# Kernel optimization log

Measured on AMD Instinct MI355X. Metric: run time of the kernel, lower is better.

The kernel has to match this reference:

```python
import jax, jax.numpy as jnp
import numpy as np

B, T, C = 32, 256, 512
MAX_LEN = 25


def setup_inputs() -> dict:
    key = jax.random.key(0)
    ks = jax.random.split(key, 6)
    scale = 1.0 / np.sqrt(C)
    return {
        "word_features": jax.random.normal(ks[0], (B, T, C), dtype=jnp.float32),
        "word_fc_w": jax.random.normal(ks[1], (C, C), dtype=jnp.float32) * scale,
        "word_fc_b": jax.random.normal(ks[2], (C,), dtype=jnp.float32) * scale,
        "pos_emb": jax.random.normal(ks[3], (MAX_LEN, C), dtype=jnp.float32),
        "atten_w": jax.random.normal(ks[4], (C,), dtype=jnp.float32) * scale,
        "atten_b": jax.random.normal(ks[5], (1,), dtype=jnp.float32) * scale,
    }


def reference(word_features, word_fc_w, word_fc_b, pos_emb, atten_w, atten_b):
    # word_fc: (b,t,c) -> (b,t,c)
    wf = jnp.einsum("btc,dc->btd", word_features, word_fc_w) + word_fc_b
    # additive (Bahdanau) attention scores over t for each of max_len query positions
    # add_features: (b, L, t, c) = wf[:,None,:,:] + pos_emb[None,:,None,:]
    add_features = jnp.tanh(wf[:, None, :, :] + pos_emb[None, :, None, :])
    # atten_fc: (b, L, t, 1) -> squeeze -> (b, L, t)
    scores = jnp.einsum("bltc,c->blt", add_features, atten_w) + atten_b[0]
    attn = jax.nn.softmax(scores, axis=2)  # softmax over t
    # bmm: (b,L,t) @ (b,t,c) -> (b,L,c)
    pvam_features = jnp.einsum("blt,btc->blc", attn, wf)
    return pvam_features
```

## Files before the change

### kernel.cpp

```cpp
#include <hip/hip_runtime.h>

#define Bn 32
#define Tn 256
#define Cn 512
#define Ln 25

typedef _Float16 h8 __attribute__((ext_vector_type(8)));
typedef _Float16 h4 __attribute__((ext_vector_type(4)));
typedef __attribute__((ext_vector_type(4))) float f32x4;

#define SCALE2LOG2E 2.885390081777927f

#if __has_builtin(__builtin_amdgcn_exp2f)
#define EXP2(x) __builtin_amdgcn_exp2f(x)
#else
#define EXP2(x) __expf(0.69314718056f * (x))
#endif

#define DPP_ADD(v, ctrl) \
    ((v) + __int_as_float(__builtin_amdgcn_update_dpp(0, __float_as_int(v), ctrl, 0xf, 0xf, true)))

__device__ __forceinline__ float tanh_fast(float x) {
    float e = EXP2(SCALE2LOG2E * x);
    return fmaf(-2.f, __builtin_amdgcn_rcpf(1.f + e), 1.f);
}

#define NA_OCT (Bn * Tn * Cn / 8)
#define NW_OCT (Cn * Cn / 8)
#define NP_OCT (Ln * Cn / 8)
__global__ __launch_bounds__(256) void k_convert(
        const float* __restrict__ A, const float* __restrict__ W,
        const float* __restrict__ pos,
        _Float16* __restrict__ A2, _Float16* __restrict__ W2,
        float* __restrict__ TP) {
    int idx = blockIdx.x * 256 + threadIdx.x;
    if (idx < NA_OCT + NW_OCT) {
        const float* src;
        _Float16* dst;
        int off;
        if (idx < NA_OCT) { src = A; dst = A2; off = idx * 8; }
        else              { src = W; dst = W2; off = (idx - NA_OCT) * 8; }
        float4 v0 = *(const float4*)&src[off];
        float4 v1 = *(const float4*)&src[off + 4];
        h8 o;
        o[0] = (_Float16)v0.x; o[1] = (_Float16)v0.y;
        o[2] = (_Float16)v0.z; o[3] = (_Float16)v0.w;
        o[4] = (_Float16)v1.x; o[5] = (_Float16)v1.y;
        o[6] = (_Float16)v1.z; o[7] = (_Float16)v1.w;
        *(h8*)&dst[off] = o;
    } else if (idx < NA_OCT + NW_OCT + NP_OCT) {
        int off = (idx - NA_OCT - NW_OCT) * 8;
        float4 v0 = *(const float4*)&pos[off];
        float4 v1 = *(const float4*)&pos[off + 4];
        float4 t0, t1;
        t0.x = tanh_fast(v0.x); t0.y = tanh_fast(v0.y);
        t0.z = tanh_fast(v0.z); t0.w = tanh_fast(v0.w);
        t1.x = tanh_fast(v1.x); t1.y = tanh_fast(v1.y);
        t1.z = tanh_fast(v1.z); t1.w = tanh_fast(v1.w);
        *(float4*)&TP[off] = t0;
        *(float4*)&TP[off + 4] = t1;
    }
}

#define BM 128
#define BN 64
#define BKg 64
__global__ __launch_bounds__(256) void k_gemm(
        const _Float16* __restrict__ A2, const _Float16* __restrict__ W2,
        const float* __restrict__ bias, _Float16* __restrict__ wf) {
    __shared__ _Float16 As[BM * BKg];
    __shared__ _Float16 Ws[BN * BKg];
    const int tid  = threadIdx.x;
    const int lane = tid & 63;
    const int wv   = tid >> 6;
    const int m0 = blockIdx.y * BM;
    const int n0 = blockIdx.x * BN;
    const int wm = (wv >> 1) * 64;
    const int wn = (wv & 1) * 32;
    const int r = lane & 15, q = lane >> 4;

    const _Float16* gA[4];
    const _Float16* gW[2];
    #pragma unroll
    for (int rr = 0; rr < 4; ++rr) {
        int p = rr * 256 + tid;
        int row = p >> 3, pk = p & 7;
        int lk = pk ^ (row & 7);
        gA[rr] = A2 + (size_t)(m0 + row) * Cn + lk * 8;
    }
    #pragma unroll
    for (int rr = 0; rr < 2; ++rr) {
        int p = rr * 256 + tid;
        int row = p >> 3, pk = p & 7;
        int lk = pk ^ (row & 7);
        gW[rr] = W2 + (size_t)(n0 + row) * Cn + lk * 8;
    }

    f32x4 acc[4][2];
    #pragma unroll
    for (int mi = 0; mi < 4; ++mi)
        #pragma unroll
        for (int ni = 0; ni < 2; ++ni) acc[mi][ni] = (f32x4){0.f, 0.f, 0.f, 0.f};

    for (int kt = 0; kt < Cn / BKg; ++kt) {
        __syncthreads();
        #pragma unroll
        for (int rr = 0; rr < 4; ++rr) {
            __builtin_amdgcn_global_load_lds(
                (const __attribute__((address_space(1))) unsigned int*)gA[rr],
                (__attribute__((address_space(3))) unsigned int*)(As + (rr * 256 + wv * 64) * 8),
                16, 0, 0);
            gA[rr] += BKg;
        }
        #pragma unroll
        for (int rr = 0; rr < 2; ++rr) {
            __builtin_amdgcn_global_load_lds(
                (const __attribute__((address_space(1))) unsigned int*)gW[rr],
                (__attribute__((address_space(3))) unsigned int*)(Ws + (rr * 256 + wv * 64) * 8),
                16, 0, 0);
            gW[rr] += BKg;
        }
        __syncthreads();

        h8 af[4][2], bfr[2][2];
        #pragma unroll
        for (int mi = 0; mi < 4; ++mi)
            #pragma unroll
            for (int kk = 0; kk < 2; ++kk) {
                int row = wm + mi * 16 + r;
                int phys = (kk * 4 + q) ^ (r & 7);
                af[mi][kk] = *(const h8*)&As[row * BKg + phys * 8];
            }
        #pragma unroll
        for (int ni = 0; ni < 2; ++ni)
            #pragma unroll
            for (int kk = 0; kk < 2; ++kk) {
                int row = wn + ni * 16 + r;
                int phys = (kk * 4 + q) ^ (r & 7);
                bfr[ni][kk] = *(const h8*)&Ws[row * BKg + phys * 8];
            }
        #pragma unroll
        for (int kk = 0; kk < 2; ++kk)
            #pragma unroll
            for (int mi = 0; mi < 4; ++mi)
                #pragma unroll
                for (int ni = 0; ni < 2; ++ni)
                    acc[mi][ni] = __builtin_amdgcn_mfma_f32_16x16x32_f16(
                        af[mi][kk], bfr[ni][kk], acc[mi][ni], 0, 0, 0);
    }

    #pragma unroll
    for (int ni = 0; ni < 2; ++ni) {
        const float bv = bias[n0 + wn + ni * 16 + r];
        #pragma unroll
        for (int mi = 0; mi < 4; ++mi)
            #pragma unroll
            for (int reg = 0; reg < 4; ++reg) {
                int row = m0 + wm + mi * 16 + q * 4 + reg;
                int col = n0 + wn + ni * 16 + r;
                wf[(size_t)row * Cn + col] = (_Float16)(acc[mi][ni][reg] + bv);
            }
    }
}

__global__ __launch_bounds__(512) void k_scores(
        const _Float16* __restrict__ wf, const float* __restrict__ TP,
        const float* __restrict__ aw, float* __restrict__ scores) {
    __shared__ float part[4 * Ln * 8];
    const int tid  = threadIdx.x;
    const int lane = tid & 63;
    const int wv   = tid >> 6;
    const int tl   = wv >> 1;
    const int ch   = wv & 1;
    const int t    = blockIdx.x * 4 + tl;
    const int b    = blockIdx.y;
    const int co   = ch * 256 + lane * 4;

    const h4 wh = *(const h4*)&wf[(size_t)(b * Tn + t) * Cn + co];
    float4 tw;
    tw.x = tanh_fast((float)wh[0]); tw.y = tanh_fast((float)wh[1]);
    tw.z = tanh_fast((float)wh[2]); tw.w = tanh_fast((float)wh[3]);
    const float4 a = *(const float4*)&aw[co];

    const float* pp = TP + co;
    float* prt = &part[tl * Ln * 8 + ch * 4 + (lane >> 4)];
    const bool writer = ((lane & 15) == 0);

    #pragma unroll
    for (int lo = 0; lo < 5; ++lo) {
        float4 pv[5];
        #pragma unroll
        for (int j = 0; j < 5; ++j)
            pv[j] = *(const float4*)(pp + (lo * 5 + j) * Cn);
        #pragma unroll
        for (int j = 0; j < 5; ++j) {
            const float4 p = pv[j];
            float s;
            {
                float d = fmaf(tw.x, p.x, 1.f);
                s = a.x * (tw.x + p.x) * __builtin_amdgcn_rcpf(d);
            }
            {
                float d = fmaf(tw.y, p.y, 1.f);
                s = fmaf(a.y * (tw.y + p.y), __builtin_amdgcn_rcpf(d), s);
            }
            {
                float d = fmaf(tw.z, p.z, 1.f);
                s = fmaf(a.z * (tw.z + p.z), __builtin_amdgcn_rcpf(d), s);
            }
            {
                float d = fmaf(tw.w, p.w, 1.f);
                s = fmaf(a.w * (tw.w + p.w), __builtin_amdgcn_rcpf(d), s);
            }
            s = DPP_ADD(s, 0xB1);
            s = DPP_ADD(s, 0x4E);
            s = DPP_ADD(s, 0x141);
            s = DPP_ADD(s, 0x140);
            if (writer) prt[(lo * 5 + j) * 8] = s;
        }
    }
    __syncthreads();
    if (tid < 4 * Ln) {
        int tl2 = tid / Ln, l2 = tid - tl2 * Ln;
        const float* q = &part[(tl2 * Ln + l2) * 8];
        float v = ((q[0] + q[1]) + (q[2] + q[3])) + ((q[4] + q[5]) + (q[6] + q[7]));
        scores[(b * Ln + l2) * Tn + blockIdx.x * 4 + tl2] = v;
    }
}

__global__ __launch_bounds__(512) void k_pvam(
        const _Float16* __restrict__ wf, const float* __restrict__ scores,
        float* __restrict__ out) {
    __shared__ float buf[8 * Ln * 64];
    __shared__ float pT[Tn][28];
    const int tid = threadIdx.x;
    const int cx  = blockIdx.x;
    const int b   = blockIdx.y;

    const float* sc = scores + b * Ln * Tn;
    for (int i = tid * 4; i < Ln * Tn; i += 2048)
        *(float4*)&buf[i] = *(const float4*)&sc[i];
    __syncthreads();

    const int lane = tid & 63;
    const int wv   = tid >> 6;

    for (int l = wv; l < Ln; l += 8) {
        float v0 = buf[l * Tn + lane];
        float v1 = buf[l * Tn + 64 + lane];
        float v2 = buf[l * Tn + 128 + lane];
        float v3 = buf[l * Tn + 192 + lane];
        float m = fmaxf(fmaxf(v0, v1), fmaxf(v2, v3));
        #pragma unroll
        for (int o = 32; o > 0; o >>= 1) m = fmaxf(m, __shfl_xor(m, o));
        float e0 = __expf(v0 - m), e1 = __expf(v1 - m);
        float e2 = __expf(v2 - m), e3 = __expf(v3 - m);
        float s = e0 + e1 + e2 + e3;
        #pragma unroll
        for (int o = 32; o > 0; o >>= 1) s += __shfl_xor(s, o);
        float rs = __builtin_amdgcn_rcpf(s);
        pT[lane][l]       = e0 * rs;
        pT[64 + lane][l]  = e1 * rs;
        pT[128 + lane][l] = e2 * rs;
        pT[192 + lane][l] = e3 * rs;
    }
    __syncthreads();

    const int c = cx * 64 + lane;
    float acc[Ln];
    #pragma unroll
    for (int l = 0; l < Ln; ++l) acc[l] = 0.f;

    const _Float16* wfp = wf + (size_t)(b * Tn + wv * 32) * Cn + c;
    for (int tt = 0; tt < 32; ++tt) {
        float w = (float)wfp[(size_t)tt * Cn];
        const float* pp = &pT[wv * 32 + tt][0];
        float p[Ln];
        *(float4*)&p[0]  = *(const float4*)&pp[0];
        *(float4*)&p[4]  = *(const float4*)&pp[4];
        *(float4*)&p[8]  = *(const float4*)&pp[8];
        *(float4*)&p[12] = *(const float4*)&pp[12];
        *(float4*)&p[16] = *(const float4*)&pp[16];
        *(float4*)&p[20] = *(const float4*)&pp[20];
        p[24] = pp[24];
        #pragma unroll
        for (int l = 0; l < Ln; ++l) acc[l] = fmaf(p[l], w, acc[l]);
    }

    __syncthreads();
    #pragma unroll
    for (int l = 0; l < Ln; ++l)
        buf[(wv * Ln + l) * 64 + lane] = acc[l];
    __syncthreads();
    for (int idx = tid; idx < Ln * 64; idx += 512) {
        int l = idx >> 6, cc = idx & 63;
        float v = 0.f;
        #pragma unroll
        for (int w = 0; w < 8; ++w) v += buf[(w * Ln + l) * 64 + cc];
        out[(b * Ln + l) * Cn + cx * 64 + cc] = v;
    }
}

extern "C" void kernel_launch(void* const* d_in, const int* in_sizes, int n_in,
                              void* d_out, int out_size, void* d_ws, size_t ws_size,
                              hipStream_t stream) {
    const float* A    = (const float*)d_in[0];
    const float* W    = (const float*)d_in[1];
    const float* bias = (const float*)d_in[2];
    const float* pos  = (const float*)d_in[3];
    const float* aw   = (const float*)d_in[4];

    char* ws = (char*)d_ws;
    _Float16*  wf     = (_Float16*)ws;
    float*     scores = (float*)(ws + 8388608ull);
    _Float16*  A2     = (_Float16*)(ws + 9240576ull);
    _Float16*  W2     = (_Float16*)(ws + 17629184ull);
    float*     TP     = (float*)(ws + 18153472ull);
    float* out = (float*)d_out;

    const int nconv = (NA_OCT + NW_OCT + NP_OCT + 255) / 256;
    k_convert<<<nconv, 256, 0, stream>>>(A, W, pos, A2, W2, TP);
    k_gemm<<<dim3(Cn / BN, (Bn * Tn) / BM), 256, 0, stream>>>(A2, W2, bias, wf);
    k_scores<<<dim3(Tn / 4, Bn), 512, 0, stream>>>(wf, TP, aw, scores);
    k_pvam<<<dim3(Cn / 64, Bn), 512, 0, stream>>>(wf, scores, out);
}
```

Baseline: 121.8 us.

## Fuse fp32-to-fp16 activation conversion into GEMM and simplify tanh-sum algebra

```diff
diff --git a/kernel.cpp b/kernel.cpp
--- a/kernel.cpp
+++ b/kernel.cpp
@@ -20,45 +20,33 @@
 #define DPP_ADD(v, ctrl) \
     ((v) + __int_as_float(__builtin_amdgcn_update_dpp(0, __float_as_int(v), ctrl, 0xf, 0xf, true)))
 
-__device__ __forceinline__ float tanh_fast(float x) {
-    float e = EXP2(SCALE2LOG2E * x);
-    return fmaf(-2.f, __builtin_amdgcn_rcpf(1.f + e), 1.f);
-}
-
-#define NA_OCT (Bn * Tn * Cn / 8)
 #define NW_OCT (Cn * Cn / 8)
 #define NP_OCT (Ln * Cn / 8)
 __global__ __launch_bounds__(256) void k_convert(
-        const float* __restrict__ A, const float* __restrict__ W,
-        const float* __restrict__ pos,
-        _Float16* __restrict__ A2, _Float16* __restrict__ W2,
-        float* __restrict__ TP) {
+        const float* __restrict__ W, const float* __restrict__ pos,
+        _Float16* __restrict__ W2, float* __restrict__ EP) {
     int idx = blockIdx.x * 256 + threadIdx.x;
-    if (idx < NA_OCT + NW_OCT) {
-        const float* src;
-        _Float16* dst;
-        int off;
-        if (idx < NA_OCT) { src = A; dst = A2; off = idx * 8; }
-        else              { src = W; dst = W2; off = (idx - NA_OCT) * 8; }
-        float4 v0 = *(const float4*)&src[off];
-        float4 v1 = *(const float4*)&src[off + 4];
+    if (idx < NW_OCT) {
+        int off = idx * 8;
+        float4 v0 = *(const float4*)&W[off];
+        float4 v1 = *(const float4*)&W[off + 4];
         h8 o;
         o[0] = (_Float16)v0.x; o[1] = (_Float16)v0.y;
         o[2] = (_Float16)v0.z; o[3] = (_Float16)v0.w;
         o[4] = (_Float16)v1.x; o[5] = (_Float16)v1.y;
         o[6] = (_Float16)v1.z; o[7] = (_Float16)v1.w;
-        *(h8*)&dst[off] = o;
-    } else if (idx < NA_OCT + NW_OCT + NP_OCT) {
-        int off = (idx - NA_OCT - NW_OCT) * 8;
+        *(h8*)&W2[off] = o;
+    } else if (idx < NW_OCT + NP_OCT) {
+        int off = (idx - NW_OCT) * 8;
         float4 v0 = *(const float4*)&pos[off];
         float4 v1 = *(const float4*)&pos[off + 4];
         float4 t0, t1;
-        t0.x = tanh_fast(v0.x); t0.y = tanh_fast(v0.y);
-        t0.z = tanh_fast(v0.z); t0.w = tanh_fast(v0.w);
-        t1.x = tanh_fast(v1.x); t1.y = tanh_fast(v1.y);
-        t1.z = tanh_fast(v1.z); t1.w = tanh_fast(v1.w);
-        *(float4*)&TP[off] = t0;
-        *(float4*)&TP[off + 4] = t1;
+        t0.x = EXP2(SCALE2LOG2E * v0.x); t0.y = EXP2(SCALE2LOG2E * v0.y);
+        t0.z = EXP2(SCALE2LOG2E * v0.z); t0.w = EXP2(SCALE2LOG2E * v0.w);
+        t1.x = EXP2(SCALE2LOG2E * v1.x); t1.y = EXP2(SCALE2LOG2E * v1.y);
+        t1.z = EXP2(SCALE2LOG2E * v1.z); t1.w = EXP2(SCALE2LOG2E * v1.w);
+        *(float4*)&EP[off] = t0;
+        *(float4*)&EP[off + 4] = t1;
     }
 }
 
@@ -66,7 +54,7 @@
 #define BN 64
 #define BKg 64
 __global__ __launch_bounds__(256) void k_gemm(
-        const _Float16* __restrict__ A2, const _Float16* __restrict__ W2,
+        const float* __restrict__ A, const _Float16* __restrict__ W2,
         const float* __restrict__ bias, _Float16* __restrict__ wf) {
     __shared__ _Float16 As[BM * BKg];
     __shared__ _Float16 Ws[BN * BKg];
@@ -79,14 +67,14 @@
     const int wn = (wv & 1) * 32;
     const int r = lane & 15, q = lane >> 4;
 
-    const _Float16* gA[4];
+    const float* gA[4];
     const _Float16* gW[2];
     #pragma unroll
     for (int rr = 0; rr < 4; ++rr) {
         int p = rr * 256 + tid;
         int row = p >> 3, pk = p & 7;
         int lk = pk ^ (row & 7);
-        gA[rr] = A2 + (size_t)(m0 + row) * Cn + lk * 8;
+        gA[rr] = A + (size_t)(m0 + row) * Cn + lk * 8;
     }
     #pragma unroll
     for (int rr = 0; rr < 2; ++rr) {
@@ -103,15 +91,14 @@
         for (int ni = 0; ni < 2; ++ni) acc[mi][ni] = (f32x4){0.f, 0.f, 0.f, 0.f};
 
     for (int kt = 0; kt < Cn / BKg; ++kt) {
-        __syncthreads();
+        float4 va[4], vb[4];
         #pragma unroll
         for (int rr = 0; rr < 4; ++rr) {
-            __builtin_amdgcn_global_load_lds(
-                (const __attribute__((address_space(1))) unsigned int*)gA[rr],
-                (__attribute__((address_space(3))) unsigned int*)(As + (rr * 256 + wv * 64) * 8),
-                16, 0, 0);
+            va[rr] = *(const float4*)gA[rr];
+            vb[rr] = *(const float4*)(gA[rr] + 4);
             gA[rr] += BKg;
         }
+        __syncthreads();
         #pragma unroll
         for (int rr = 0; rr < 2; ++rr) {
             __builtin_amdgcn_global_load_lds(
@@ -120,6 +107,15 @@
                 16, 0, 0);
             gW[rr] += BKg;
         }
+        #pragma unroll
+        for (int rr = 0; rr < 4; ++rr) {
+            h8 o;
+            o[0] = (_Float16)va[rr].x; o[1] = (_Float16)va[rr].y;
+            o[2] = (_Float16)va[rr].z; o[3] = (_Float16)va[rr].w;
+            o[4] = (_Float16)vb[rr].x; o[5] = (_Float16)vb[rr].y;
+            o[6] = (_Float16)vb[rr].z; o[7] = (_Float16)vb[rr].w;
+            *(h8*)&As[(rr * 256 + tid) * 8] = o;
+        }
         __syncthreads();
 
         h8 af[4][2], bfr[2][2];
@@ -164,7 +160,7 @@
 }
 
 __global__ __launch_bounds__(512) void k_scores(
-        const _Float16* __restrict__ wf, const float* __restrict__ TP,
+        const _Float16* __restrict__ wf, const float* __restrict__ EP,
         const float* __restrict__ aw, float* __restrict__ scores) {
     __shared__ float part[4 * Ln * 8];
     const int tid  = threadIdx.x;
@@ -177,12 +173,15 @@
     const int co   = ch * 256 + lane * 4;
 
     const h4 wh = *(const h4*)&wf[(size_t)(b * Tn + t) * Cn + co];
-    float4 tw;
-    tw.x = tanh_fast((float)wh[0]); tw.y = tanh_fast((float)wh[1]);
-    tw.z = tanh_fast((float)wh[2]); tw.w = tanh_fast((float)wh[3]);
-    const float4 a = *(const float4*)&aw[co];
-
-    const float* pp = TP + co;
+    float4 ew;
+    ew.x = EXP2(SCALE2LOG2E * (float)wh[0]);
+    ew.y = EXP2(SCALE2LOG2E * (float)wh[1]);
+    ew.z = EXP2(SCALE2LOG2E * (float)wh[2]);
+    ew.w = EXP2(SCALE2LOG2E * (float)wh[3]);
+    float4 a = *(const float4*)&aw[co];
+    a.x *= -2.f; a.y *= -2.f; a.z *= -2.f; a.w *= -2.f;
+
+    const float* pp = EP + co;
     float* prt = &part[tl * Ln * 8 + ch * 4 + (lane >> 4)];
     const bool writer = ((lane & 15) == 0);
 
@@ -195,23 +194,14 @@
         #pragma unroll
         for (int j = 0; j < 5; ++j) {
             const float4 p = pv[j];
-            float s;
-            {
-                float d = fmaf(tw.x, p.x, 1.f);
-                s = a.x * (tw.x + p.x) * __builtin_amdgcn_rcpf(d);
-            }
-            {
-                float d = fmaf(tw.y, p.y, 1.f);
-                s = fmaf(a.y * (tw.y + p.y), __builtin_amdgcn_rcpf(d), s);
-            }
-            {
-                float d = fmaf(tw.z, p.z, 1.f);
-                s = fmaf(a.z * (tw.z + p.z), __builtin_amdgcn_rcpf(d), s);
-            }
-            {
-                float d = fmaf(tw.w, p.w, 1.f);
-                s = fmaf(a.w * (tw.w + p.w), __builtin_amdgcn_rcpf(d), s);
-            }
+            float d0 = fmaf(ew.x, p.x, 1.f);
+            float s  = a.x * __builtin_amdgcn_rcpf(d0);
+            float d1 = fmaf(ew.y, p.y, 1.f);
+            s = fmaf(a.y, __builtin_amdgcn_rcpf(d1), s);
+            float d2 = fmaf(ew.z, p.z, 1.f);
+            s = fmaf(a.z, __builtin_amdgcn_rcpf(d2), s);
+            float d3 = fmaf(ew.w, p.w, 1.f);
+            s = fmaf(a.w, __builtin_amdgcn_rcpf(d3), s);
             s = DPP_ADD(s, 0xB1);
             s = DPP_ADD(s, 0x4E);
             s = DPP_ADD(s, 0x141);
@@ -313,14 +303,13 @@
     char* ws = (char*)d_ws;
     _Float16*  wf     = (_Float16*)ws;
     float*     scores = (float*)(ws + 8388608ull);
-    _Float16*  A2     = (_Float16*)(ws + 9240576ull);
-    _Float16*  W2     = (_Float16*)(ws + 17629184ull);
-    float*     TP     = (float*)(ws + 18153472ull);
+    _Float16*  W2     = (_Float16*)(ws + 9207808ull);
+    float*     EP     = (float*)(ws + 9732096ull);
     float* out = (float*)d_out;
 
-    const int nconv = (NA_OCT + NW_OCT + NP_OCT + 255) / 256;
-    k_convert<<<nconv, 256, 0, stream>>>(A, W, pos, A2, W2, TP);
-    k_gemm<<<dim3(Cn / BN, (Bn * Tn) / BM), 256, 0, stream>>>(A2, W2, bias, wf);
-    k_scores<<<dim3(Tn / 4, Bn), 512, 0, stream>>>(wf, TP, aw, scores);
+    const int nconv = (NW_OCT + NP_OCT + 255) / 256;
+    k_convert<<<nconv, 256, 0, stream>>>(W, pos, W2, EP);
+    k_gemm<<<dim3(Cn / BN, (Bn * Tn) / BM), 256, 0, stream>>>(A, W2, bias, wf);
+    k_scores<<<dim3(Tn / 4, Bn), 512, 0, stream>>>(wf, EP, aw, scores);
     k_pvam<<<dim3(Cn / 64, Bn), 512, 0, stream>>>(wf, scores, out);
 }
```

New measurement: 123.0 us. Within noise of the previous version (+0.9%).
